# Optimization experiments

Measured on AMD Instinct MI355X. Metric: run time of the kernel, lower is better.

Reference implementation:

```python
import jax, jax.numpy as jnp
import numpy as np


def setup_inputs() -> dict:
    key = jax.random.key(0)
    k1, k2, k3 = jax.random.split(key, 3)
    B, T, N, D = 16, 12, 4096, 64
    M = 128  # memory_num
    return {
        "nodevec1": jax.random.normal(k1, (B, T, N, D), dtype=jnp.float32),
        "nodevec2": jax.random.normal(k2, (B, T, N, D), dtype=jnp.float32),
        "node_embeddings": jax.random.normal(k3, (M, 2 * D), dtype=jnp.float32),
        "topk": 32,
    }


def reference(nodevec1, nodevec2, node_embeddings, topk):
    B, T, N, D = nodevec1.shape
    M = node_embeddings.shape[0]
    # nodevec3: [B,T,N,2D] matches node_embeddings' 2*time_dim trailing dim
    nodevec3 = jnp.concatenate([nodevec1, nodevec2], axis=-1)
    # attention-like map over nodes: [B,T,M,N]
    logits = jnp.einsum('me,btne->btmn', node_embeddings, nodevec3)
    supports2 = jax.nn.softmax(logits, axis=-1)
    values, indices = jax.lax.top_k(supports2, topk)  # [B,T,M,K], sorted desc

    def gather(x):
        # gather K nodes per memory slot along the N axis
        idx = indices.reshape(B, T, M * topk, 1)  # [B,T,M*K,1]
        g = jnp.take_along_axis(x, idx, axis=2)   # [B,T,M*K,D]
        return g.reshape(B, T, M, topk, D)

    sel1 = gather(nodevec1)
    sel2 = gather(nodevec2)
    batch_indices = jnp.broadcast_to(jnp.arange(B).reshape(B, 1, 1, 1), (B, T, M, topk))
    time_indices = jnp.broadcast_to(jnp.arange(T).reshape(1, T, 1, 1), (B, T, M, topk))
    return (sel1, sel2, batch_indices, time_indices, indices)
```

## Files before the change

### kernel.cpp

```cpp
#include <hip/hip_runtime.h>
#include <stdint.h>

typedef unsigned long long u64;
typedef unsigned short u16;
typedef __attribute__((ext_vector_type(8))) short short8;
typedef __attribute__((ext_vector_type(4))) float f32x4;

#define NB   16
#define NT   12
#define BTc  192
#define NN   4096
#define DD   64
#define MM   128
#define TOPK 32
#define KTH  36
#define DLT  2.0f
#define CAP  128

#define SEL1_OFF 0ULL
#define SEL2_OFF 50331648ULL
#define BIDX_OFF 100663296ULL
#define TIDX_OFF 101449728ULL
#define IDX_OFF  102236160ULL

__device__ __forceinline__ unsigned ord32(float f) {
    unsigned u = __float_as_uint(f);
    return (u & 0x80000000u) ? ~u : (u | 0x80000000u);
}
__device__ __forceinline__ u16 f2bf(float f) {
    unsigned u = __float_as_uint(f);
    unsigned r = u + 0x7FFFu + ((u >> 16) & 1u);
    return (u16)(r >> 16);
}
__device__ __forceinline__ float bf2f(short s) {
    return __uint_as_float(((unsigned)(u16)s) << 16);
}
__device__ __forceinline__ u64 pack4bf(float4 v) {
    return (u64)f2bf(v.x) | ((u64)f2bf(v.y) << 16) |
           ((u64)f2bf(v.z) << 32) | ((u64)f2bf(v.w) << 48);
}
__device__ __forceinline__ void lds_fence() {
    asm volatile("s_waitcnt lgkmcnt(0)" ::: "memory");
    __builtin_amdgcn_sched_barrier(0);
}
__device__ __forceinline__ float sort64f_desc(float v, int l) {
#pragma unroll
    for (int k = 2; k <= 64; k <<= 1) {
#pragma unroll
        for (int j = k >> 1; j >= 1; j >>= 1) {
            float o = __shfl_xor(v, j);
            bool takeMax = (((l & j) == 0) == ((l & k) == 0));
            v = takeMax ? fmaxf(v, o) : fminf(v, o);
        }
    }
    return v;
}
__device__ __forceinline__ u64 sort64_desc(u64 v, int l) {
#pragma unroll
    for (int k = 2; k <= 64; k <<= 1) {
#pragma unroll
        for (int j = k >> 1; j >= 1; j >>= 1) {
            u64 o = __shfl_xor(v, j);
            bool takeMax = (((l & j) == 0) == ((l & k) == 0));
            v = takeMax ? (v > o ? v : o) : (v < o ? v : o);
        }
    }
    return v;
}

__global__ __launch_bounds__(256) void k1_logits_bf16(const float* __restrict__ nv1,
                                                      const float* __restrict__ nv2,
                                                      const float* __restrict__ emb,
                                                      u16* __restrict__ logitsB) {
    __shared__ u16 S[2 * 128 * 128];
    u16* Als = S;
    u16* Bls = S + 128 * 128;

    const int tid = threadIdx.x;
    const int nt  = blockIdx.x;
    const int bt  = blockIdx.y;
    const int n0  = nt * 128;

#pragma unroll
    for (int it = 0; it < 16; ++it) {
        int f4  = it * 256 + tid;
        int row = f4 >> 5;
        int kq  = f4 & 31;
        float4 a = *(const float4*)(emb + row * 128 + kq * 4);
        int byte = row * 256 + ((kq * 8) ^ ((row & 7) << 4));
        *(u64*)((char*)Als + byte) = pack4bf(a);
    }
#pragma unroll
    for (int it = 0; it < 16; ++it) {
        int f4  = it * 256 + tid;
        int row = f4 >> 5;
        int kq  = f4 & 31;
        const float* src = (kq < 16)
            ? (nv1 + ((size_t)bt * NN + n0 + row) * DD + kq * 4)
            : (nv2 + ((size_t)bt * NN + n0 + row) * DD + (kq - 16) * 4);
        float4 bv = *(const float4*)src;
        int byte = row * 256 + ((kq * 8) ^ ((row & 7) << 4));
        *(u64*)((char*)Bls + byte) = pack4bf(bv);
    }
    __syncthreads();

    const int w  = tid >> 6;
    const int l  = tid & 63;
    const int mb = (w >> 1) * 64;
    const int nb = (w & 1) * 64;
    const int xr = (l & 7) << 4;

    f32x4 acc[4][4];
#pragma unroll
    for (int mi = 0; mi < 4; ++mi)
#pragma unroll
        for (int ni = 0; ni < 4; ++ni) acc[mi][ni] = {0.f, 0.f, 0.f, 0.f};

#pragma unroll
    for (int ks = 0; ks < 4; ++ks) {
        const int kb = (ks * 64 + (l >> 4) * 16) ^ xr;
        short8 a[4], b[4];
#pragma unroll
        for (int mi = 0; mi < 4; ++mi) {
            int row = mb + mi * 16 + (l & 15);
            a[mi] = *(const short8*)((const char*)Als + row * 256 + kb);
        }
#pragma unroll
        for (int ni = 0; ni < 4; ++ni) {
            int row = nb + ni * 16 + (l & 15);
            b[ni] = *(const short8*)((const char*)Bls + row * 256 + kb);
        }
#pragma unroll
        for (int mi = 0; mi < 4; ++mi)
#pragma unroll
            for (int ni = 0; ni < 4; ++ni)
                acc[mi][ni] = __builtin_amdgcn_mfma_f32_16x16x32_bf16(
                    a[mi], b[ni], acc[mi][ni], 0, 0, 0);
    }

    __syncthreads();
#pragma unroll
    for (int mi = 0; mi < 4; ++mi) {
#pragma unroll
        for (int ni = 0; ni < 4; ++ni) {
#pragma unroll
            for (int r = 0; r < 4; ++r) {
                int m   = mb + mi * 16 + (l >> 4) * 4 + r;
                int col = nb + ni * 16 + (l & 15);
                int byte = m * 256 + ((col * 2) ^ (((m >> 2) & 3) << 5));
                *(u16*)((char*)S + byte) = f2bf(acc[mi][ni][r]);
            }
        }
    }
    __syncthreads();

    const size_t rbase = (size_t)bt * MM * NN;
#pragma unroll
    for (int it = 0; it < 8; ++it) {
        int f    = it * 256 + tid;
        int m    = f >> 4;
        int ck   = f & 15;
        int byte = m * 256 + ((ck * 16) ^ (((m >> 2) & 3) << 5));
        f32x4 v  = *(const f32x4*)((const char*)S + byte);
        *(f32x4*)(logitsB + rbase + (size_t)m * NN + n0 + ck * 8) = v;
    }
}

__global__ __launch_bounds__(256) void k2_fused(const u16* logitsB,
                                                const float* __restrict__ nv1,
                                                const float* __restrict__ nv2,
                                                const float* __restrict__ emb,
                                                float* out) {
    const int tid = threadIdx.x;
    const int l   = tid & 63;
    const int w   = tid >> 6;
    const int bid = (int)blockIdx.x;
    const int swz = (bid & 7) * 768 + (bid >> 3);
    const int row = swz * 4 + w;
    const int bt  = row >> 7;
    const int m   = row & 127;
    const u16* src = logitsB + (size_t)row * NN;

    __shared__ int   cand[4][CAP];
    __shared__ float embrow[4][128];

    embrow[w][l]      = emb[m * 128 + l];
    embrow[w][l + 64] = emb[m * 128 + 64 + l];

    short8 ch[8];
#pragma unroll
    for (int j = 0; j < 8; ++j)
        ch[j] = *(const short8*)(src + j * 512 + l * 8);

    float lmax = -INFINITY;
#pragma unroll
    for (int j = 0; j < 8; ++j)
#pragma unroll
        for (int e = 0; e < 8; ++e) lmax = fmaxf(lmax, bf2f(ch[j][e]));

    const float T = __shfl(sort64f_desc(lmax, l), KTH - 1);

    int c = 0;
    const u64 below = (1ull << l) - 1ull;
#pragma unroll
    for (int j = 0; j < 8; ++j) {
#pragma unroll
        for (int e = 0; e < 8; ++e) {
            bool p = (bf2f(ch[j][e]) >= T);
            u64 mask = __ballot(p);
            if (p) {
                int pos = c + (int)__popcll(mask & below);
                if (pos < CAP)
                    cand[w][pos] = ((int)(u16)ch[j][e] << 16) | (j * 512 + l * 8 + e);
            }
            c += (int)__popcll(mask);
        }
    }
    if (c > CAP) c = CAP;
    lds_fence();

    {
        int rd0 = (l < c)      ? cand[w][l]      : 0;
        int rd1 = (l + 64 < c) ? cand[w][l + 64] : 0;
        float a0 = (l < c)      ? bf2f((short)(u16)((unsigned)rd0 >> 16)) : -INFINITY;
        float a1 = (l + 64 < c) ? bf2f((short)(u16)((unsigned)rd1 >> 16)) : -INFINITY;
        const float V32 = __shfl(sort64f_desc(a0, l), 31);
        const float thr = V32 - DLT;
        bool k0  = (l < c)      && (a0 >= thr);
        bool k1b = (l + 64 < c) && (a1 >= thr);
        u64 mk0 = __ballot(k0);
        u64 mk1 = __ballot(k1b);
        int base1 = (int)__popcll(mk0);
        if (k0)  cand[w][(int)__popcll(mk0 & below)]         = rd0;
        if (k1b) cand[w][base1 + (int)__popcll(mk1 & below)] = rd1;
        c = base1 + (int)__popcll(mk1);
        lds_fence();
    }

    u64 kreg[2] = {0ull, 0ull};
    const int nch = (c + 63) >> 6;
    for (int s3 = 0; s3 < nch; ++s3) {
        int s = s3 * 64 + l;
        if (s < c) {
            int n = cand[w][s] & 0xFFFF;
            const float4* c1 = (const float4*)(nv1 + ((size_t)bt * NN + n) * DD);
            const float4* c2 = (const float4*)(nv2 + ((size_t)bt * NN + n) * DD);
            float acc = 0.f;
#pragma unroll
            for (int q = 0; q < 16; ++q) {
                float4 x = c1[q];
                acc = fmaf(embrow[w][q * 4 + 0], x.x, acc);
                acc = fmaf(embrow[w][q * 4 + 1], x.y, acc);
                acc = fmaf(embrow[w][q * 4 + 2], x.z, acc);
                acc = fmaf(embrow[w][q * 4 + 3], x.w, acc);
            }
#pragma unroll
            for (int q = 0; q < 16; ++q) {
                float4 x = c2[q];
                acc = fmaf(embrow[w][64 + q * 4 + 0], x.x, acc);
                acc = fmaf(embrow[w][64 + q * 4 + 1], x.y, acc);
                acc = fmaf(embrow[w][64 + q * 4 + 2], x.z, acc);
                acc = fmaf(embrow[w][64 + q * 4 + 3], x.w, acc);
            }
            kreg[s3] = ((u64)ord32(acc) << 32) | (u64)(0xFFFFFFFFu - (unsigned)n);
        }
    }

    u64 top = sort64_desc(kreg[0], l);
    if (c > 64) {
        u64 Bk = sort64_desc(kreg[1], l);
        u64 rb = __shfl_xor(Bk, 63);
        u64 M = top > rb ? top : rb;
#pragma unroll
        for (int j = 32; j >= 1; j >>= 1) {
            u64 o = __shfl_xor(M, j);
            M = ((l & j) == 0) ? (M > o ? M : o) : (M < o ? M : o);
        }
        top = M;
    }

    const int b = bt / NT;
    const int t = bt - b * NT;
    const size_t obase = (size_t)row * TOPK;
    const unsigned mynode = 0xFFFFFFFFu - (unsigned)(top & 0xFFFFFFFFull);
    if (l < TOPK) {
        out[IDX_OFF  + obase + l] = (float)mynode;
        out[BIDX_OFF + obase + l] = (float)b;
        out[TIDX_OFF + obase + l] = (float)t;
    }

    int myn[8];
#pragma unroll
    for (int it = 0; it < 8; ++it) {
        int p = it * 4 + (l >> 4);
        u64 kk = __shfl(top, p);
        myn[it] = (int)(0xFFFFFFFFu - (unsigned)(kk & 0xFFFFFFFFull)) & (NN - 1);
    }
    const int j4 = (l & 15) * 4;
#pragma unroll
    for (int it = 0; it < 8; ++it) {
        int p = it * 4 + (l >> 4);
        const float4 s1 = *(const float4*)(nv1 + ((size_t)bt * NN + myn[it]) * DD + j4);
        const float4 s2 = *(const float4*)(nv2 + ((size_t)bt * NN + myn[it]) * DD + j4);
        size_t o = (obase + p) * DD + j4;
        *(float4*)(out + SEL1_OFF + o) = s1;
        *(float4*)(out + SEL2_OFF + o) = s2;
    }
}

extern "C" void kernel_launch(void* const* d_in, const int* in_sizes, int n_in,
                              void* d_out, int out_size, void* d_ws, size_t ws_size,
                              hipStream_t stream) {
    const float* nv1 = (const float*)d_in[0];
    const float* nv2 = (const float*)d_in[1];
    const float* emb = (const float*)d_in[2];
    float* out = (float*)d_out;

    dim3 g1(32, BTc);
    k1_logits_bf16<<<g1, 256, 0, stream>>>(nv1, nv2, emb, (u16*)d_out);
    k2_fused<<<24576 / 4, 256, 0, stream>>>((const u16*)d_out, nv1, nv2, emb, out);
}
```

Baseline: 376.4 us.

## Process each top-k row with a full 256-thread block instead of one wave

The fused selection kernel now assigns one logits row per 256-thread block rather than one row per wave, and launches four times as many blocks. Each thread scans 16 bf16 logits, the per-wave sorted maxima are merged through shared memory to find the threshold, and candidates are compacted with a shared atomic counter. Exact fp32 rescoring is spread across all four waves, and the gather of the selected rows uses all 256 threads. The second-stage delta pruning of candidates is dropped, so more candidates may be rescored, and the extra __syncthreads barriers and shared-memory atomics add overhead.

```diff
diff --git a/kernel.cpp b/kernel.cpp
--- a/kernel.cpp
+++ b/kernel.cpp
@@ -14,7 +14,6 @@
 #define MM   128
 #define TOPK 32
 #define KTH  36
-#define DLT  2.0f
 #define CAP  128
 
 #define SEL1_OFF 0ULL
@@ -39,10 +38,6 @@
     return (u64)f2bf(v.x) | ((u64)f2bf(v.y) << 16) |
            ((u64)f2bf(v.z) << 32) | ((u64)f2bf(v.w) << 48);
 }
-__device__ __forceinline__ void lds_fence() {
-    asm volatile("s_waitcnt lgkmcnt(0)" ::: "memory");
-    __builtin_amdgcn_sched_barrier(0);
-}
 __device__ __forceinline__ float sort64f_desc(float v, int l) {
 #pragma unroll
     for (int k = 2; k <= 64; k <<= 1) {
@@ -52,6 +47,16 @@
             bool takeMax = (((l & j) == 0) == ((l & k) == 0));
             v = takeMax ? fmaxf(v, o) : fminf(v, o);
         }
+    }
+    return v;
+}
+__device__ __forceinline__ float merge64f_desc(float a, float b, int l) {
+    float rb = __shfl_xor(b, 63);
+    float v = fmaxf(a, rb);
+#pragma unroll
+    for (int j = 32; j >= 1; j >>= 1) {
+        float o = __shfl_xor(v, j);
+        v = ((l & j) == 0) ? fmaxf(v, o) : fminf(v, o);
     }
     return v;
 }
@@ -175,136 +180,123 @@
     const int l   = tid & 63;
     const int w   = tid >> 6;
     const int bid = (int)blockIdx.x;
-    const int swz = (bid & 7) * 768 + (bid >> 3);
-    const int row = swz * 4 + w;
+    const int row = (bid & 7) * 3072 + (bid >> 3);
     const int bt  = row >> 7;
     const int m   = row & 127;
     const u16* src = logitsB + (size_t)row * NN;
 
-    __shared__ int   cand[4][CAP];
-    __shared__ float embrow[4][128];
-
-    embrow[w][l]      = emb[m * 128 + l];
-    embrow[w][l + 64] = emb[m * 128 + 64 + l];
-
-    short8 ch[8];
-#pragma unroll
-    for (int j = 0; j < 8; ++j)
-        ch[j] = *(const short8*)(src + j * 512 + l * 8);
-
-    float lmax = -INFINITY;
-#pragma unroll
-    for (int j = 0; j < 8; ++j)
-#pragma unroll
-        for (int e = 0; e < 8; ++e) lmax = fmaxf(lmax, bf2f(ch[j][e]));
-
-    const float T = __shfl(sort64f_desc(lmax, l), KTH - 1);
-
-    int c = 0;
+    __shared__ float sortedW[4][64];
+    __shared__ float embrow[128];
+    __shared__ int   cand[CAP];
+    __shared__ u64   keyL[CAP];
+    __shared__ int   widx[TOPK];
+    __shared__ int   cnt;
+    __shared__ float Tsh;
+
+    if (tid < 128) embrow[tid] = emb[m * 128 + tid];
+    if (tid < CAP) keyL[tid] = 0ull;
+    if (tid == 0)  cnt = 0;
+
+    const short8 c0 = *(const short8*)(src + tid * 16);
+    const short8 c1 = *(const short8*)(src + tid * 16 + 8);
+    float tmax = -INFINITY;
+#pragma unroll
+    for (int e = 0; e < 8; ++e) tmax = fmaxf(tmax, bf2f(c0[e]));
+#pragma unroll
+    for (int e = 0; e < 8; ++e) tmax = fmaxf(tmax, bf2f(c1[e]));
+
+    sortedW[w][l] = sort64f_desc(tmax, l);
+    __syncthreads();
+
+    if (w == 0) {
+        float m01 = merge64f_desc(sortedW[0][l], sortedW[1][l], l);
+        float m23 = merge64f_desc(sortedW[2][l], sortedW[3][l], l);
+        float top = merge64f_desc(m01, m23, l);
+        if (l == KTH - 1) Tsh = top;
+    }
+    __syncthreads();
+    const float T = Tsh;
+
     const u64 below = (1ull << l) - 1ull;
 #pragma unroll
-    for (int j = 0; j < 8; ++j) {
-#pragma unroll
-        for (int e = 0; e < 8; ++e) {
-            bool p = (bf2f(ch[j][e]) >= T);
-            u64 mask = __ballot(p);
-            if (p) {
-                int pos = c + (int)__popcll(mask & below);
-                if (pos < CAP)
-                    cand[w][pos] = ((int)(u16)ch[j][e] << 16) | (j * 512 + l * 8 + e);
+    for (int e = 0; e < 16; ++e) {
+        float v = bf2f((e < 8) ? c0[e] : c1[e - 8]);
+        bool p = (v >= T);
+        u64 mask = __ballot(p);
+        int nw = (int)__popcll(mask);
+        int base = 0;
+        if (l == 0 && nw) base = atomicAdd(&cnt, nw);
+        base = __shfl(base, 0);
+        if (p) {
+            int pos = base + (int)__popcll(mask & below);
+            if (pos < CAP) cand[pos] = tid * 16 + e;
+        }
+    }
+    __syncthreads();
+    const int c = (cnt < CAP) ? cnt : CAP;
+
+    {
+        const int i = (l << 2) | w;
+        if (i < c) {
+            int n = cand[i];
+            const float4* p1 = (const float4*)(nv1 + ((size_t)bt * NN + n) * DD);
+            const float4* p2 = (const float4*)(nv2 + ((size_t)bt * NN + n) * DD);
+            float acc = 0.f;
+#pragma unroll
+            for (int q = 0; q < 16; ++q) {
+                float4 x = p1[q];
+                acc = fmaf(embrow[q * 4 + 0], x.x, acc);
+                acc = fmaf(embrow[q * 4 + 1], x.y, acc);
+                acc = fmaf(embrow[q * 4 + 2], x.z, acc);
+                acc = fmaf(embrow[q * 4 + 3], x.w, acc);
             }
-            c += (int)__popcll(mask);
-        }
-    }
-    if (c > CAP) c = CAP;
-    lds_fence();
-
-    {
-        int rd0 = (l < c)      ? cand[w][l]      : 0;
-        int rd1 = (l + 64 < c) ? cand[w][l + 64] : 0;
-        float a0 = (l < c)      ? bf2f((short)(u16)((unsigned)rd0 >> 16)) : -INFINITY;
-        float a1 = (l + 64 < c) ? bf2f((short)(u16)((unsigned)rd1 >> 16)) : -INFINITY;
-        const float V32 = __shfl(sort64f_desc(a0, l), 31);
-        const float thr = V32 - DLT;
-        bool k0  = (l < c)      && (a0 >= thr);
-        bool k1b = (l + 64 < c) && (a1 >= thr);
-        u64 mk0 = __ballot(k0);
-        u64 mk1 = __ballot(k1b);
-        int base1 = (int)__popcll(mk0);
-        if (k0)  cand[w][(int)__popcll(mk0 & below)]         = rd0;
-        if (k1b) cand[w][base1 + (int)__popcll(mk1 & below)] = rd1;
-        c = base1 + (int)__popcll(mk1);
-        lds_fence();
-    }
-
-    u64 kreg[2] = {0ull, 0ull};
-    const int nch = (c + 63) >> 6;
-    for (int s3 = 0; s3 < nch; ++s3) {
-        int s = s3 * 64 + l;
-        if (s < c) {
-            int n = cand[w][s] & 0xFFFF;
-            const float4* c1 = (const float4*)(nv1 + ((size_t)bt * NN + n) * DD);
-            const float4* c2 = (const float4*)(nv2 + ((size_t)bt * NN + n) * DD);
-            float acc = 0.f;
 #pragma unroll
             for (int q = 0; q < 16; ++q) {
-                float4 x = c1[q];
-                acc = fmaf(embrow[w][q * 4 + 0], x.x, acc);
-                acc = fmaf(embrow[w][q * 4 + 1], x.y, acc);
-                acc = fmaf(embrow[w][q * 4 + 2], x.z, acc);
-                acc = fmaf(embrow[w][q * 4 + 3], x.w, acc);
+                float4 x = p2[q];
+                acc = fmaf(embrow[64 + q * 4 + 0], x.x, acc);
+                acc = fmaf(embrow[64 + q * 4 + 1], x.y, acc);
+                acc = fmaf(embrow[64 + q * 4 + 2], x.z, acc);
+                acc = fmaf(embrow[64 + q * 4 + 3], x.w, acc);
             }
-#pragma unroll
-            for (int q = 0; q < 16; ++q) {
-                float4 x = c2[q];
-                acc = fmaf(embrow[w][64 + q * 4 + 0], x.x, acc);
-                acc = fmaf(embrow[w][64 + q * 4 + 1], x.y, acc);
-                acc = fmaf(embrow[w][64 + q * 4 + 2], x.z, acc);
-                acc = fmaf(embrow[w][64 + q * 4 + 3], x.w, acc);
-            }
-            kreg[s3] = ((u64)ord32(acc) << 32) | (u64)(0xFFFFFFFFu - (unsigned)n);
-        }
-    }
-
-    u64 top = sort64_desc(kreg[0], l);
-    if (c > 64) {
-        u64 Bk = sort64_desc(kreg[1], l);
-        u64 rb = __shfl_xor(Bk, 63);
-        u64 M = top > rb ? top : rb;
+            keyL[i] = ((u64)ord32(acc) << 32) | (u64)(0xFFFFFFFFu - (unsigned)n);
+        }
+    }
+    __syncthreads();
+
+    const size_t obase = (size_t)row * TOPK;
+    if (w == 0) {
+        u64 A  = sort64_desc(keyL[l], l);
+        u64 Bs = sort64_desc(keyL[64 + l], l);
+        u64 rb = __shfl_xor(Bs, 63);
+        u64 M  = A > rb ? A : rb;
 #pragma unroll
         for (int j = 32; j >= 1; j >>= 1) {
             u64 o = __shfl_xor(M, j);
             M = ((l & j) == 0) ? (M > o ? M : o) : (M < o ? M : o);
         }
-        top = M;
-    }
-
-    const int b = bt / NT;
-    const int t = bt - b * NT;
-    const size_t obase = (size_t)row * TOPK;
-    const unsigned mynode = 0xFFFFFFFFu - (unsigned)(top & 0xFFFFFFFFull);
-    if (l < TOPK) {
-        out[IDX_OFF  + obase + l] = (float)mynode;
-        out[BIDX_OFF + obase + l] = (float)b;
-        out[TIDX_OFF + obase + l] = (float)t;
-    }
-
-    int myn[8];
-#pragma unroll
-    for (int it = 0; it < 8; ++it) {
-        int p = it * 4 + (l >> 4);
-        u64 kk = __shfl(top, p);
-        myn[it] = (int)(0xFFFFFFFFu - (unsigned)(kk & 0xFFFFFFFFull)) & (NN - 1);
-    }
-    const int j4 = (l & 15) * 4;
-#pragma unroll
-    for (int it = 0; it < 8; ++it) {
-        int p = it * 4 + (l >> 4);
-        const float4 s1 = *(const float4*)(nv1 + ((size_t)bt * NN + myn[it]) * DD + j4);
-        const float4 s2 = *(const float4*)(nv2 + ((size_t)bt * NN + myn[it]) * DD + j4);
-        size_t o = (obase + p) * DD + j4;
-        *(float4*)(out + SEL1_OFF + o) = s1;
-        *(float4*)(out + SEL2_OFF + o) = s2;
+        const unsigned node = 0xFFFFFFFFu - (unsigned)(M & 0xFFFFFFFFull);
+        if (l < TOPK) {
+            const int b = bt / NT;
+            out[IDX_OFF  + obase + l] = (float)node;
+            out[BIDX_OFF + obase + l] = (float)b;
+            out[TIDX_OFF + obase + l] = (float)(bt - b * NT);
+            widx[l] = (int)node & (NN - 1);
+        }
+    }
+    __syncthreads();
+
+#pragma unroll
+    for (int it = 0; it < 4; ++it) {
+        int id = it * 256 + tid;
+        int p  = id >> 5;
+        int ck = id & 31;
+        int j  = ck & 15;
+        bool h2 = ck >= 16;
+        int n = widx[p];
+        const float* basep = h2 ? nv2 : nv1;
+        float4 sv = *(const float4*)(basep + ((size_t)bt * NN + n) * DD + j * 4);
+        size_t o = (obase + p) * DD + j * 4;
+        *(float4*)(out + (h2 ? SEL2_OFF : SEL1_OFF) + o) = sv;
     }
 }
 
@@ -318,5 +310,5 @@
 
     dim3 g1(32, BTc);
     k1_logits_bf16<<<g1, 256, 0, stream>>>(nv1, nv2, emb, (u16*)d_out);
-    k2_fused<<<24576 / 4, 256, 0, stream>>>((const u16*)d_out, nv1, nv2, emb, out);
-}
+    k2_fused<<<24576, 256, 0, stream>>>((const u16*)d_out, nv1, nv2, emb, out);
+}
```

Result: no change. 383.8 us (+2.0%).
